# Optimization experiments

Measured on AMD Instinct MI355X. Metric: run time of the kernel, lower is better.

## Reference

```python
import jax, jax.numpy as jnp
import numpy as np

HEADS = 16
NUM_LANDMARKS = 64
PINV_ITERS = 6
D_MODEL = 1024


def _moore_penrose_pinv(x, num_iters):
    # Newton-Schulz iteration: V <- 0.25*V @ (13I - KV @ (15I - KV @ (7I - KV)))
    m = x.shape[-1]
    I = jnp.eye(m, dtype=x.dtype)
    V = x
    for _ in range(num_iters):
        KV = x @ V  # [..., m, m]
        V = 0.25 * V @ (13.0 * I - KV @ (15.0 * I - KV @ (7.0 * I - KV)))
    return V


def setup_inputs() -> dict:
    key = jax.random.key(0)
    k1, k2, k3 = jax.random.split(key, 3)
    b, n, d = 4, 4096, D_MODEL
    hidden_states = jax.random.normal(k1, (b, n, d), dtype=jnp.float32)
    Wqkv = jax.random.normal(k2, (d, 3 * d), dtype=jnp.float32) * 0.02
    bqkv = jnp.zeros((3 * d,), dtype=jnp.float32)
    Wout = jax.random.normal(k3, (d, d), dtype=jnp.float32) * 0.02
    bout = jnp.zeros((d,), dtype=jnp.float32)
    return {"hidden_states": hidden_states, "Wqkv": Wqkv, "bqkv": bqkv,
            "Wout": Wout, "bout": bout}


def reference(hidden_states, Wqkv, bqkv, Wout, bout):
    b, n, d = hidden_states.shape
    h, m = HEADS, NUM_LANDMARKS
    dh = d // h
    scale = 1.0 / np.sqrt(dh).astype(np.float32)
    # n is a multiple of m by construction, so the torch padding branch is a no-op.
    l = n // m  # tokens per landmark group

    qkv = hidden_states @ Wqkv + bqkv  # [b, n, 3d]
    q, k, v = jnp.split(qkv, 3, axis=-1)

    def to_heads(t):  # [b, n, d] -> [b, h, n, dh]
        return t.reshape(b, n, h, dh).transpose(0, 2, 1, 3)

    q, k, v = to_heads(q), to_heads(k), to_heads(v)
    q = q * scale

    # Landmarks: mean over contiguous groups of l tokens (sum / l in original).
    q_l = q.reshape(b, h, m, l, dh).mean(axis=3)  # [b, h, m, dh]
    k_l = k.reshape(b, h, m, l, dh).mean(axis=3)

    sim1 = jnp.einsum('bhid,bhjd->bhij', q, k_l)    # [b, h, n, m]
    sim2 = jnp.einsum('bhid,bhjd->bhij', q_l, k_l)  # [b, h, m, m]
    sim3 = jnp.einsum('bhid,bhjd->bhij', q_l, k)    # [b, h, m, n]

    attn1 = jax.nn.softmax(sim1, axis=-1)
    attn2 = jax.nn.softmax(sim2, axis=-1)
    attn3 = jax.nn.softmax(sim3, axis=-1)

    attn2_inv = _moore_penrose_pinv(attn2, PINV_ITERS)

    # out = attn1 @ attn2_inv @ (attn3 @ v), cheapest association
    out = attn1 @ (attn2_inv @ (attn3 @ v))  # [b, h, n, dh]
    out = out.transpose(0, 2, 1, 3).reshape(b, n, d)
    out = out @ Wout + bout
    return out
```

## Files before the change

kernel.cpp:

```cpp
#include <hip/hip_runtime.h>
#include <cstdint>

typedef unsigned short u16;
typedef __attribute__((ext_vector_type(8))) short s16x8;
typedef __attribute__((ext_vector_type(4))) float f32x4;

#define NTOK 4096
#define DH   64
#define DM   1024
#define NH   16

static __device__ __forceinline__ float b2f(u16 u){ return __uint_as_float(((unsigned)u)<<16); }
static __device__ __forceinline__ u16 f2b(float f){
  unsigned u = __float_as_uint(f);
  return (u16)((u + 0x7FFFu + ((u>>16)&1u)) >> 16);
}

static __device__ __forceinline__ void gload_lds16(const void* g, void* l) {
  __builtin_amdgcn_global_load_lds(
      (const __attribute__((address_space(1))) unsigned*)(uintptr_t)g,
      (__attribute__((address_space(3))) unsigned*)(uintptr_t)l, 16, 0, 0);
}

static __device__ __forceinline__ s16x8 ld8(const u16* p){ return *(const s16x8*)(const void*)p; }

__global__ __launch_bounds__(256) void k_cvt_xl(const float* __restrict__ hs, u16* __restrict__ Xb,
                                                float* __restrict__ Xl) {
  const int grp = blockIdx.x;
  const int d = blockIdx.y*256 + threadIdx.x;
  const float* p = hs + (long)grp*64*DM + d;
  u16* xo = Xb + (long)grp*64*DM + d;
  float s = 0.f;
  #pragma unroll 8
  for (int i = 0; i < 64; ++i) {
    const float v = p[(long)i*DM];
    s += v;
    xo[(long)i*DM] = f2b(v);
  }
  Xl[(long)grp*DM + d] = s * (1.0f/64.0f);
}

__global__ __launch_bounds__(256) void k_cvt_t(const float* __restrict__ in, u16* __restrict__ out, int R, int C) {
  __shared__ float tile[64][65];
  const int tc = blockIdx.x, tr = blockIdx.y;
  const int t = threadIdx.x, cx = t & 63, ry = t >> 6;
  #pragma unroll
  for (int p = 0; p < 16; ++p) {
    const int row = p*4 + ry;
    tile[row][cx] = in[(long)(tr*64 + row)*C + tc*64 + cx];
  }
  __syncthreads();
  #pragma unroll
  for (int p = 0; p < 16; ++p) {
    const int orow = p*4 + ry;
    out[(long)(tc*64 + orow)*R + tr*64 + cx] = f2b(tile[cx][orow]);
  }
}

__global__ __launch_bounds__(256) void k_lproj2(const float* __restrict__ Xl, const float* __restrict__ Wqkv,
                                                float* __restrict__ psum) {
  __shared__ __align__(16) float Xs[32][68];
  const int t = threadIdx.x;
  const int wcol = blockIdx.x*256 + t;
  const int r0 = blockIdx.y*32;
  const int kbase = blockIdx.z*128;
  float acc[32];
  #pragma unroll
  for (int r = 0; r < 32; ++r) acc[r] = 0.f;
  for (int k0 = kbase; k0 < kbase + 128; k0 += 64) {
    __syncthreads();
    for (int idx = t; idx < 2048; idx += 256)
      Xs[idx>>6][idx&63] = Xl[(long)(r0 + (idx>>6))*DM + k0 + (idx&63)];
    __syncthreads();
    for (int kk = 0; kk < 64; kk += 4) {
      f32x4 wv;
      #pragma unroll
      for (int j = 0; j < 4; ++j) wv[j] = Wqkv[(long)(k0+kk+j)*3072 + wcol];
      #pragma unroll
      for (int r = 0; r < 32; ++r) {
        const f32x4 xv = *(const f32x4*)&Xs[r][kk];
        acc[r] += xv[0]*wv[0] + xv[1]*wv[1] + xv[2]*wv[2] + xv[3]*wv[3];
      }
    }
  }
  float* po = psum + ((long)blockIdx.z*256 + r0)*2048 + wcol;
  #pragma unroll
  for (int r = 0; r < 32; ++r) po[(long)r*2048] = acc[r];
}

__global__ __launch_bounds__(256) void k_lreduce(const float* __restrict__ psum, const float* __restrict__ bqkv,
                                                 float* __restrict__ qlf, float* __restrict__ klf,
                                                 u16* __restrict__ qlb, u16* __restrict__ klb) {
  const long idx = (long)blockIdx.x*256 + threadIdx.x;
  const int row = (int)(idx >> 11), col = (int)(idx & 2047);
  float s = 0.f;
  #pragma unroll
  for (int z = 0; z < 8; ++z) s += psum[((long)z*256 + row)*2048 + col];
  const int isq = (col < 1024) ? 1 : 0;
  float val = s + bqkv[col];
  if (isq) val *= 0.125f;
  const int b = row >> 6, lm = row & 63;
  const int c2 = col & 1023, h = c2 >> 6, dh = c2 & 63;
  const long o = (((long)b*NH + h)*64 + lm)*64 + dh;
  if (isq) { qlf[o] = val; qlb[o] = f2b(val); }
  else     { klf[o] = val; klb[o] = f2b(val); }
}

template<int EPI>
__global__ __launch_bounds__(512, 2) void k_gemm256(
    const u16* __restrict__ A, const u16* __restrict__ Bt, const float* __restrict__ bias,
    int N, float* __restrict__ outF, u16* __restrict__ outQ, u16* __restrict__ outK, u16* __restrict__ outV)
{
  __shared__ __align__(16) u16 lds[4*16384];
  const int K = 1024;
  const int t = threadIdx.x;
  const int lane = t & 63;
  const int wid = t >> 6;
  const int c = lane & 15, g = lane >> 4;
  const int wm = wid >> 2, wn = wid & 3;
  const int fid = blockIdx.y*64 + blockIdx.x;
  const int nbx = ((fid & 7) << 3) | ((fid >> 3) & 7);
  const int nby = fid >> 6;
  const long arow0 = (long)nbx * 256;
  const long brow0 = (long)nby * 256;
  char* ldsb = (char*)lds;

  const int srow = t >> 2;
  const int schunk = (t & 3) ^ ((srow >> 1) & 3);
  const u16* gA0 = A  + (arow0 + srow)*K       + schunk*8;
  const u16* gA1 = A  + (arow0 + 128 + srow)*K + schunk*8;
  const u16* gB0 = Bt + (brow0 + srow)*K       + schunk*8;
  const u16* gB1 = Bt + (brow0 + 128 + srow)*K + schunk*8;
  const int dstoff = t*16;

#define STAGE_A(kt) { char* bse = ldsb + ((kt)&3)*32768; \
    gload_lds16(gA0 + (kt)*32, bse + dstoff); \
    gload_lds16(gA1 + (kt)*32, bse + 8192 + dstoff); }
#define STAGE_B(kt) { char* bse = ldsb + ((kt)&3)*32768 + 16384; \
    gload_lds16(gB0 + (kt)*32, bse + dstoff); \
    gload_lds16(gB1 + (kt)*32, bse + 8192 + dstoff); }

  const int gs = g ^ ((c >> 1) & 3);
  int aoff[2][4], boff[4];
  #pragma unroll
  for (int mi = 0; mi < 4; ++mi) {
    aoff[0][mi] = (0*128 + wm*64 + mi*16 + c)*64 + gs*16;
    aoff[1][mi] = (1*128 + wm*64 + mi*16 + c)*64 + gs*16;
    boff[mi]    = 16384 + (wn*64 + mi*16 + c)*64 + gs*16;
  }

  f32x4 acc0[4][4] = {};
  f32x4 acc1[4][4] = {};

  STAGE_A(0); STAGE_B(0); STAGE_A(1); STAGE_B(1); STAGE_A(2); STAGE_B(2);
  asm volatile("s_waitcnt vmcnt(8)" ::: "memory");
  __builtin_amdgcn_s_barrier();

  s16x8 af[4], bfr[4], af2[4];
  #pragma unroll
  for (int mi = 0; mi < 4; ++mi) af[mi]  = *(const s16x8*)(ldsb + aoff[0][mi]);
  #pragma unroll
  for (int ni = 0; ni < 4; ++ni) bfr[ni] = *(const s16x8*)(ldsb + boff[ni]);

  for (int kt = 0; kt < 32; ++kt) {
    char* buf  = ldsb + (kt&3)*32768;
    char* bufn = ldsb + ((kt+1)&3)*32768;
    if (kt + 3 < 32) { STAGE_A(kt+3) STAGE_B(kt+3) }
    asm volatile("s_waitcnt lgkmcnt(0)" ::: "memory");
    __builtin_amdgcn_sched_barrier(0);
    #pragma unroll
    for (int mi = 0; mi < 4; ++mi) af2[mi] = *(const s16x8*)(buf + aoff[1][mi]);
    __builtin_amdgcn_sched_barrier(0);
    __builtin_amdgcn_s_setprio(1);
    #pragma unroll
    for (int mi = 0; mi < 4; ++mi)
      #pragma unroll
      for (int ni = 0; ni < 4; ++ni)
        acc0[mi][ni] = __builtin_amdgcn_mfma_f32_16x16x32_bf16(af[mi], bfr[ni], acc0[mi][ni], 0, 0, 0);
    __builtin_amdgcn_s_setprio(0);
    asm volatile("s_waitcnt lgkmcnt(0)" ::: "memory");
    __builtin_amdgcn_sched_barrier(0);
    if (kt <= 28)      { asm volatile("s_waitcnt vmcnt(8)" ::: "memory"); }
    else if (kt == 29) { asm volatile("s_waitcnt vmcnt(4)" ::: "memory"); }
    else if (kt == 30) { asm volatile("s_waitcnt vmcnt(0)" ::: "memory"); }
    if (kt < 31) __builtin_amdgcn_s_barrier();
    s16x8 nf[4], nb[4];
    if (kt < 31) {
      #pragma unroll
      for (int mi = 0; mi < 4; ++mi) nf[mi] = *(const s16x8*)(bufn + aoff[0][mi]);
      #pragma unroll
      for (int ni = 0; ni < 4; ++ni) nb[ni] = *(const s16x8*)(bufn + boff[ni]);
    }
    __builtin_amdgcn_sched_barrier(0);
    __builtin_amdgcn_s_setprio(1);
    #pragma unroll
    for (int mi = 0; mi < 4; ++mi)
      #pragma unroll
      for (int ni = 0; ni < 4; ++ni)
        acc1[mi][ni] = __builtin_amdgcn_mfma_f32_16x16x32_bf16(af2[mi], bfr[ni], acc1[mi][ni], 0, 0, 0);
    __builtin_amdgcn_s_setprio(0);
    if (kt < 31) {
      #pragma unroll
      for (int mi = 0; mi < 4; ++mi) { af[mi] = nf[mi]; bfr[mi] = nb[mi]; }
    }
  }
#undef STAGE_A
#undef STAGE_B

  if (EPI == 0) {
    const int tensor = (int)(brow0 >> 10);
    u16* dst = (tensor == 0) ? outQ : (tensor == 1) ? outK : outV;
    const float mul = (tensor == 0) ? 0.125f : 1.0f;
    #pragma unroll
    for (int ph = 0; ph < 2; ++ph)
      #pragma unroll
      for (int mi = 0; mi < 4; ++mi) {
        const int rowb = ph*128 + wm*64 + mi*16 + g*4;
        #pragma unroll
        for (int ni = 0; ni < 4; ++ni) {
          const long gcol = brow0 + wn*64 + ni*16 + c;
          const int c2 = (int)(gcol & 1023);
          const int head = c2 >> 6, dh = c2 & 63;
          const float bv = bias[gcol];
          const f32x4 a = ph ? acc1[mi][ni] : acc0[mi][ni];
          #pragma unroll
          for (int r = 0; r < 4; ++r) {
            const long grow = arow0 + rowb + r;
            const int b = (int)(grow >> 12), tok = (int)(grow & 4095);
            dst[(((long)b*NH + head)*NTOK + tok)*DH + dh] = f2b((a[r] + bv)*mul);
          }
        }
      }
  } else {
    #pragma unroll
    for (int ph = 0; ph < 2; ++ph)
      #pragma unroll
      for (int mi = 0; mi < 4; ++mi) {
        const int rowb = ph*128 + wm*64 + mi*16 + g*4;
        #pragma unroll
        for (int ni = 0; ni < 4; ++ni) {
          const long gcol = brow0 + wn*64 + ni*16 + c;
          const float bv = bias[gcol];
          const f32x4 a = ph ? acc1[mi][ni] : acc0[mi][ni];
          #pragma unroll
          for (int r = 0; r < 4; ++r) {
            const long grow = arow0 + rowb + r;
            outF[grow*N + gcol] = a[r] + bv;
          }
        }
      }
  }
}

__global__ __launch_bounds__(256) void k_vtrans(const u16* __restrict__ v, u16* __restrict__ vt) {
  __shared__ u16 tile[64][65];
  const int bh = blockIdx.x >> 6, tt = blockIdx.x & 63;
  const int t = threadIdx.x, cx = t & 63, ry = t >> 6;
  const u16* vp = v + ((long)bh*NTOK + tt*64)*DH;
  #pragma unroll
  for (int p = 0; p < 16; ++p) { const int row = p*4 + ry; tile[row][cx] = vp[row*DH + cx]; }
  __syncthreads();
  u16* op = vt + (long)bh*DH*NTOK + tt*64;
  #pragma unroll
  for (int p = 0; p < 16; ++p) { const int orow = p*4 + ry; op[(long)orow*NTOK + cx] = tile[cx][orow]; }
}

#define PST 68
static __device__ __forceinline__ void mm_nn8(const float* A, const float* B, float* C, int t) {
  const int lane = t & 63, j0 = (t >> 6) << 3;
  float acc[8];
  #pragma unroll
  for (int j = 0; j < 8; ++j) acc[j] = 0.f;
  for (int k = 0; k < 64; k += 4) {
    const f32x4 a4 = *(const f32x4*)&A[lane*PST + k];
    #pragma unroll
    for (int dk = 0; dk < 4; ++dk) {
      const float a = a4[dk];
      const float* br = &B[(k + dk)*PST + j0];
      const f32x4 b0 = *(const f32x4*)(br);
      const f32x4 b1 = *(const f32x4*)(br + 4);
      #pragma unroll
      for (int qq = 0; qq < 4; ++qq) { acc[qq] += a*b0[qq]; acc[4+qq] += a*b1[qq]; }
    }
  }
  #pragma unroll
  for (int j = 0; j < 8; ++j) C[lane*PST + j0 + j] = acc[j];
}
static __device__ __forceinline__ void mm_nt8(const float* A, const float* B, float* C, int t) {
  const int lane = t & 63, j0 = (t >> 6) << 3;
  float acc[8];
  #pragma unroll
  for (int j = 0; j < 8; ++j) acc[j] = 0.f;
  for (int k = 0; k < 64; k += 4) {
    const f32x4 a4 = *(const f32x4*)&A[lane*PST + k];
    #pragma unroll
    for (int jj = 0; jj < 8; ++jj) {
      const f32x4 b4 = *(const f32x4*)&B[(j0 + jj)*PST + k];
      acc[jj] += a4[0]*b4[0] + a4[1]*b4[1] + a4[2]*b4[2] + a4[3]*b4[3];
    }
  }
  #pragma unroll
  for (int j = 0; j < 8; ++j) C[lane*PST + j0 + j] = acc[j];
}

__global__ __launch_bounds__(512) void k_pinv(const float* __restrict__ qlf, const float* __restrict__ klf,
                                              float* __restrict__ a2inv) {
  __shared__ __align__(16) float Xb[64*PST];
  __shared__ __align__(16) float Vb[64*PST];
  __shared__ __align__(16) float T1[64*PST];
  __shared__ __align__(16) float T2[64*PST];
  __shared__ __align__(16) float T3[64*PST];
  const int bh = blockIdx.x, t = threadIdx.x;
  const float* ql = qlf + (long)bh*4096;
  const float* kl = klf + (long)bh*4096;
  for (int i = t; i < 4096; i += 512) { T1[(i>>6)*PST + (i&63)] = ql[i]; T2[(i>>6)*PST + (i&63)] = kl[i]; }
  __syncthreads();
  mm_nt8(T1, T2, Xb, t);
  __syncthreads();
  if (t < 64) {
    float mx = -1e30f;
    for (int j = 0; j < 64; ++j) mx = fmaxf(mx, Xb[t*PST + j]);
    float s = 0.f;
    for (int j = 0; j < 64; ++j) { const float e = expf(Xb[t*PST + j] - mx); Xb[t*PST + j] = e; s += e; }
    const float inv = 1.0f/s;
    for (int j = 0; j < 64; ++j) Xb[t*PST + j] *= inv;
  }
  __syncthreads();
  for (int i = t; i < 4096; i += 512) { const int r = i>>6, cc = i&63; Vb[r*PST+cc] = Xb[r*PST+cc]; }
  __syncthreads();
  for (int it = 0; it < 6; ++it) {
    mm_nn8(Xb, Vb, T1, t);  __syncthreads();
    for (int i = t; i < 4096; i += 512) { const int r=i>>6, cc=i&63; T2[r*PST+cc] = (r==cc?7.0f:0.0f) - T1[r*PST+cc]; }
    __syncthreads();
    mm_nn8(T1, T2, T3, t);  __syncthreads();
    for (int i = t; i < 4096; i += 512) { const int r=i>>6, cc=i&63; T2[r*PST+cc] = (r==cc?15.0f:0.0f) - T3[r*PST+cc]; }
    __syncthreads();
    mm_nn8(T1, T2, T3, t);  __syncthreads();
    for (int i = t; i < 4096; i += 512) { const int r=i>>6, cc=i&63; T2[r*PST+cc] = (r==cc?13.0f:0.0f) - T3[r*PST+cc]; }
    __syncthreads();
    mm_nn8(Vb, T2, T3, t);  __syncthreads();
    for (int i = t; i < 4096; i += 512) { const int r=i>>6, cc=i&63; Vb[r*PST+cc] = 0.25f*T3[r*PST+cc]; }
    __syncthreads();
  }
  for (int i = t; i < 4096; i += 512) a2inv[(long)bh*4096 + i] = Vb[(i>>6)*PST + (i&63)];
}

__global__ __launch_bounds__(256) void k_attn3v_p(const u16* __restrict__ qlb, const u16* __restrict__ kk,
                                                  const u16* __restrict__ vt,
                                                  float* __restrict__ zp, float* __restrict__ sp) {
  __shared__ __align__(16) float Zl[4][64][64];
  __shared__ float Sl[4][64];
  __shared__ __align__(16) u16 Pl[4][64][40];
  const int bh = blockIdx.x >> 2, qt = blockIdx.x & 3;
  const int t = threadIdx.x, w = t >> 6, lane = t & 63;
  const int c = lane & 15, g = lane >> 4;

  s16x8 aq[4][2];
  const u16* qlp = qlb + (long)bh*4096;
  #pragma unroll
  for (int mi = 0; mi < 4; ++mi)
    #pragma unroll
    for (int ks = 0; ks < 2; ++ks)
      aq[mi][ks] = ld8(qlp + (mi*16 + c)*64 + ks*32 + g*8);

  f32x4 zacc[4][4] = {};
  float sl[4][4] = {};
  const u16* kp = kk + (long)bh*NTOK*DH;
  const u16* vp = vt + (long)bh*DH*NTOK;
  char* pbase = (char*)&Pl[w][0][0];
  const int tok00 = qt*1024 + w*256;

  for (int it = 0; it < 8; ++it) {
    const int t0 = tok00 + it*32;
    f32x4 sacc[4][2] = {};
    s16x8 kb[2][2];
    #pragma unroll
    for (int cg = 0; cg < 2; ++cg)
      #pragma unroll
      for (int ks = 0; ks < 2; ++ks)
        kb[cg][ks] = ld8(kp + (long)(t0 + cg*16 + c)*64 + ks*32 + g*8);
    #pragma unroll
    for (int cg = 0; cg < 2; ++cg)
      #pragma unroll
      for (int ks = 0; ks < 2; ++ks)
        #pragma unroll
        for (int mi = 0; mi < 4; ++mi)
          sacc[mi][cg] = __builtin_amdgcn_mfma_f32_16x16x32_bf16(aq[mi][ks], kb[cg][ks], sacc[mi][cg], 0, 0, 0);
    #pragma unroll
    for (int mi = 0; mi < 4; ++mi)
      #pragma unroll
      for (int r = 0; r < 4; ++r) {
        const int row = mi*16 + g*4 + r;
        const float p0 = __expf(sacc[mi][0][r]);
        const float p1 = __expf(sacc[mi][1][r]);
        sl[mi][r] += p0 + p1;
        char* base = pbase + row*80;
        *(u16*)(base + c*2)      = f2b(p0);
        *(u16*)(base + 32 + c*2) = f2b(p1);
      }
    s16x8 pa[4];
    #pragma unroll
    for (int mi = 0; mi < 4; ++mi) pa[mi] = *(const s16x8*)(pbase + (mi*16 + c)*80 + g*16);
    #pragma unroll
    for (int ni = 0; ni < 4; ++ni) {
      const s16x8 vb = ld8(vp + (long)(ni*16 + c)*NTOK + t0 + g*8);
      #pragma unroll
      for (int mi = 0; mi < 4; ++mi)
        zacc[mi][ni] = __builtin_amdgcn_mfma_f32_16x16x32_bf16(pa[mi], vb, zacc[mi][ni], 0, 0, 0);
    }
  }
  #pragma unroll
  for (int mi = 0; mi < 4; ++mi)
    #pragma unroll
    for (int r = 0; r < 4; ++r) {
      float s = sl[mi][r];
      s += __shfl_xor(s, 1); s += __shfl_xor(s, 2); s += __shfl_xor(s, 4); s += __shfl_xor(s, 8);
      sl[mi][r] = s;
    }
  #pragma unroll
  for (int mi = 0; mi < 4; ++mi)
    #pragma unroll
    for (int ni = 0; ni < 4; ++ni)
      #pragma unroll
      for (int r = 0; r < 4; ++r)
        Zl[w][mi*16 + g*4 + r][ni*16 + c] = zacc[mi][ni][r];
  if (c == 0)
    #pragma unroll
    for (int mi = 0; mi < 4; ++mi)
      #pragma unroll
      for (int r = 0; r < 4; ++r)
        Sl[w][mi*16 + g*4 + r] = sl[mi][r];
  __syncthreads();
  float* zpp = zp + (long)blockIdx.x*4096;
  for (int i = t; i < 4096; i += 256) {
    const int row = i >> 6, dh = i & 63;
    zpp[i] = Zl[0][row][dh] + Zl[1][row][dh] + Zl[2][row][dh] + Zl[3][row][dh];
  }
  if (t < 64) sp[(long)blockIdx.x*64 + t] = Sl[0][t] + Sl[1][t] + Sl[2][t] + Sl[3][t];
}

__global__ __launch_bounds__(512) void k_w2(const float* __restrict__ a2inv,
                                            const float* __restrict__ zp, const float* __restrict__ sp,
                                            u16* __restrict__ w2t) {
  __shared__ __align__(16) float Ai[64*PST];
  __shared__ __align__(16) float Zi[64*PST];
  __shared__ __align__(16) float Ci[64*PST];
  __shared__ float Ss[64];
  const int bh = blockIdx.x, t = threadIdx.x;
  if (t < 64) {
    float ss = 0.f;
    #pragma unroll
    for (int qt = 0; qt < 4; ++qt) ss += sp[(long)(bh*4 + qt)*64 + t];
    Ss[t] = 1.0f / ss;
  }
  for (int i = t; i < 4096; i += 512)
    Ai[(i>>6)*PST + (i&63)] = a2inv[(long)bh*4096 + i];
  __syncthreads();
  for (int i = t; i < 4096; i += 512) {
    float zs = 0.f;
    #pragma unroll
    for (int qt = 0; qt < 4; ++qt) zs += zp[((long)(bh*4 + qt))*4096 + i];
    Zi[(i>>6)*PST + (i&63)] = zs * Ss[i>>6];
  }
  __syncthreads();
  mm_nn8(Ai, Zi, Ci, t);
  __syncthreads();
  for (int i = t; i < 4096; i += 512) { const int r = i>>6, cc = i&63; w2t[(long)bh*4096 + cc*64 + r] = f2b(Ci[r*PST + cc]); }
}

#define P1ST 144
__global__ __launch_bounds__(256) void k_attn1(const u16* __restrict__ q, const u16* __restrict__ klb,
                                               const u16* __restrict__ w2t, u16* __restrict__ ao) {
  __shared__ __align__(16) u16 Pl[4][64][72];
  const int bx = blockIdx.x, bh = bx >> 4, tt = bx & 15;
  const int b = bh >> 4, h = bh & 15;
  const int t = threadIdx.x, w = t >> 6, lane = t & 63;
  const int c = lane & 15, g = lane >> 4;
  const int tok0 = tt*256 + w*64;
  const u16* qp  = q + ((long)bh*NTOK + tok0)*DH;
  const u16* klp = klb + (long)bh*4096;
  const u16* wp  = w2t + (long)bh*4096;
  char* pbase = (char*)&Pl[w][0][0];

  s16x8 aq[4][2], kb[4][2], wb[4][2];
  #pragma unroll
  for (int i = 0; i < 4; ++i)
    #pragma unroll
    for (int ks = 0; ks < 2; ++ks) {
      aq[i][ks] = ld8(qp + (long)(i*16 + c)*DH + ks*32 + g*8);
      kb[i][ks] = ld8(klp + (i*16 + c)*64 + ks*32 + g*8);
      wb[i][ks] = ld8(wp  + (i*16 + c)*64 + ks*32 + g*8);
    }
  f32x4 sacc[4][4] = {};
  #pragma unroll
  for (int ks = 0; ks < 2; ++ks)
    #pragma unroll
    for (int mi = 0; mi < 4; ++mi)
      #pragma unroll
      for (int ni = 0; ni < 4; ++ni)
        sacc[mi][ni] = __builtin_amdgcn_mfma_f32_16x16x32_bf16(aq[mi][ks], kb[ni][ks], sacc[mi][ni], 0, 0, 0);

  float rs[4][4];
  #pragma unroll
  for (int mi = 0; mi < 4; ++mi)
    #pragma unroll
    for (int r = 0; r < 4; ++r) {
      const int row = mi*16 + g*4 + r;
      char* base = pbase + row*P1ST;
      float ssum = 0.f;
      #pragma unroll
      for (int ni = 0; ni < 4; ++ni) {
        const float p = __expf(sacc[mi][ni][r]);
        ssum += p;
        *(u16*)(base + (ni*16 + c)*2) = f2b(p);
      }
      ssum += __shfl_xor(ssum, 1); ssum += __shfl_xor(ssum, 2);
      ssum += __shfl_xor(ssum, 4); ssum += __shfl_xor(ssum, 8);
      rs[mi][r] = ssum;
    }
  __builtin_amdgcn_s_barrier();
  s16x8 pa[4][2];
  #pragma unroll
  for (int mi = 0; mi < 4; ++mi)
    #pragma unroll
    for (int ks = 0; ks < 2; ++ks)
      pa[mi][ks] = *(const s16x8*)(pbase + (mi*16 + c)*P1ST + ks*64 + g*16);
  f32x4 oacc[4][4] = {};
  #pragma unroll
  for (int ks = 0; ks < 2; ++ks)
    #pragma unroll
    for (int mi = 0; mi < 4; ++mi)
      #pragma unroll
      for (int ni = 0; ni < 4; ++ni)
        oacc[mi][ni] = __builtin_amdgcn_mfma_f32_16x16x32_bf16(pa[mi][ks], wb[ni][ks], oacc[mi][ni], 0, 0, 0);

  u16* op = ao + (long)b*NTOK*DM + (long)h*64;
  #pragma unroll
  for (int mi = 0; mi < 4; ++mi)
    #pragma unroll
    for (int r = 0; r < 4; ++r) {
      const int tok = tok0 + mi*16 + g*4 + r;
      const float inv = 1.0f / rs[mi][r];
      #pragma unroll
      for (int ni = 0; ni < 4; ++ni)
        op[(long)tok*DM + ni*16 + c] = f2b(oacc[mi][ni][r] * inv);
    }
}

extern "C" void kernel_launch(void* const* d_in, const int* in_sizes, int n_in,
                              void* d_out, int out_size, void* d_ws, size_t ws_size,
                              hipStream_t stream) {
  const float* hs   = (const float*)d_in[0];
  const float* Wqkv = (const float*)d_in[1];
  const float* bqkv = (const float*)d_in[2];
  const float* Wout = (const float*)d_in[3];
  const float* bout = (const float*)d_in[4];
  float* out = (float*)d_out;
  char* w = (char*)d_ws;

  u16*  Xb    = (u16*)(w);
  float* zp   = (float*)(w);
  float* sp   = (float*)(w + 4194304L);
  u16*  WqkvT = (u16*)(w + 33554432L);
  u16*  WoutT = (u16*)(w + 39845888L);
  u16*  q     = (u16*)(w + 41943040L);
  float* psum = (float*)(w + 41943040L);
  u16*  k     = (u16*)(w + 75497472L);
  u16*  v     = (u16*)(w + 109051904L);
  u16*  vt    = (u16*)(w + 142606336L);
  float* Xl   = (float*)(w + 142606336L);
  float* qlf  = (float*)(w + 176160768L);
  float* klf  = (float*)(w + 177209344L);
  u16*  qlb   = (u16*)(w + 178257920L);
  u16*  klb   = (u16*)(w + 178782208L);
  float* a2i  = (float*)(w + 179306496L);
  u16*  w2t   = (u16*)(w + 181403648L);
  u16*  ao    = (u16*)(w + 181927936L);

  k_cvt_xl<<<dim3(256,4), 256, 0, stream>>>(hs, Xb, Xl);
  k_cvt_t<<<dim3(48,16), 256, 0, stream>>>(Wqkv, WqkvT, 1024, 3072);
  k_cvt_t<<<dim3(16,16), 256, 0, stream>>>(Wout, WoutT, 1024, 1024);
  k_lproj2<<<dim3(8,8,8), 256, 0, stream>>>(Xl, Wqkv, psum);
  k_lreduce<<<2048, 256, 0, stream>>>(psum, bqkv, qlf, klf, qlb, klb);
  k_gemm256<0><<<dim3(64,12), 512, 0, stream>>>(Xb, WqkvT, bqkv, 3072, nullptr, q, k, v);
  k_vtrans<<<4096, 256, 0, stream>>>(v, vt);
  k_pinv<<<64, 512, 0, stream>>>(qlf, klf, a2i);
  k_attn3v_p<<<256, 256, 0, stream>>>(qlb, k, vt, zp, sp);
  k_w2<<<64, 512, 0, stream>>>(a2i, zp, sp, w2t);
  k_attn1<<<1024, 256, 0, stream>>>(q, klb, w2t, ao);
  k_gemm256<1><<<dim3(64,4), 512, 0, stream>>>(ao, WoutT, bout, 1024, out, nullptr, nullptr, nullptr);
}
```

Measured before the change: 367.6 us.

## Fuse preprocessing kernels, write V transposed from GEMM, co-schedule pinv with attn3

Merges the hidden-state conversion and both weight transposes into one launch. The QKV GEMM epilogue now writes V already transposed through LDS, which removes the separate transpose kernel and one round trip of V through memory. The pinv blocks and a finer-split attn3·V pass (8 token chunks per head) now share one launch, so the serial pinv work overlaps with the attention reduction. k_w2 is widened to 1024 threads to match. This adds LDS pressure and branch divergence between block roles, and the pinv blocks still set the critical path.

```diff
diff --git a/kernel.cpp b/kernel.cpp
--- a/kernel.cpp
+++ b/kernel.cpp
@@ -24,26 +24,31 @@
 
 static __device__ __forceinline__ s16x8 ld8(const u16* p){ return *(const s16x8*)(const void*)p; }
 
-__global__ __launch_bounds__(256) void k_cvt_xl(const float* __restrict__ hs, u16* __restrict__ Xb,
-                                                float* __restrict__ Xl) {
-  const int grp = blockIdx.x;
-  const int d = blockIdx.y*256 + threadIdx.x;
-  const float* p = hs + (long)grp*64*DM + d;
-  u16* xo = Xb + (long)grp*64*DM + d;
-  float s = 0.f;
-  #pragma unroll 8
-  for (int i = 0; i < 64; ++i) {
-    const float v = p[(long)i*DM];
-    s += v;
-    xo[(long)i*DM] = f2b(v);
-  }
-  Xl[(long)grp*DM + d] = s * (1.0f/64.0f);
-}
-
-__global__ __launch_bounds__(256) void k_cvt_t(const float* __restrict__ in, u16* __restrict__ out, int R, int C) {
+__global__ __launch_bounds__(256) void k_pre(const float* __restrict__ hs, u16* __restrict__ Xb,
+                                             float* __restrict__ Xl,
+                                             const float* __restrict__ Wqkv, u16* __restrict__ WqkvT,
+                                             const float* __restrict__ Wout, u16* __restrict__ WoutT) {
   __shared__ float tile[64][65];
-  const int tc = blockIdx.x, tr = blockIdx.y;
-  const int t = threadIdx.x, cx = t & 63, ry = t >> 6;
+  const int bid = blockIdx.x, t = threadIdx.x;
+  if (bid < 1024) {
+    const int grp = bid >> 2;
+    const int d = (bid & 3)*256 + t;
+    const float* p = hs + (long)grp*64*DM + d;
+    u16* xo = Xb + (long)grp*64*DM + d;
+    float s = 0.f;
+    #pragma unroll 8
+    for (int i = 0; i < 64; ++i) {
+      const float v = p[(long)i*DM];
+      s += v;
+      xo[(long)i*DM] = f2b(v);
+    }
+    Xl[(long)grp*DM + d] = s * (1.0f/64.0f);
+    return;
+  }
+  const float* in; u16* out; int R, C, tc, tr;
+  if (bid < 1792) { const int x = bid - 1024; in = Wqkv; out = WqkvT; R = 1024; C = 3072; tc = x % 48; tr = x / 48; }
+  else            { const int x = bid - 1792; in = Wout; out = WoutT; R = 1024; C = 1024; tc = x & 15;  tr = x >> 4; }
+  const int cx = t & 63, ry = t >> 6;
   #pragma unroll
   for (int p = 0; p < 16; ++p) {
     const int row = p*4 + ry;
@@ -209,28 +214,62 @@
 
   if (EPI == 0) {
     const int tensor = (int)(brow0 >> 10);
-    u16* dst = (tensor == 0) ? outQ : (tensor == 1) ? outK : outV;
-    const float mul = (tensor == 0) ? 0.125f : 1.0f;
-    #pragma unroll
-    for (int ph = 0; ph < 2; ++ph)
-      #pragma unroll
-      for (int mi = 0; mi < 4; ++mi) {
-        const int rowb = ph*128 + wm*64 + mi*16 + g*4;
-        #pragma unroll
-        for (int ni = 0; ni < 4; ++ni) {
-          const long gcol = brow0 + wn*64 + ni*16 + c;
-          const int c2 = (int)(gcol & 1023);
-          const int head = c2 >> 6, dh = c2 & 63;
-          const float bv = bias[gcol];
-          const f32x4 a = ph ? acc1[mi][ni] : acc0[mi][ni];
+    if (tensor == 2) {
+      __syncthreads();
+      u16* wlds = lds + wid*4224;
+      const int hbase = (int)((brow0 + wn*64) & 1023);
+      const int head = hbase >> 6;
+      #pragma unroll
+      for (int ph = 0; ph < 2; ++ph) {
+        const long grow0 = arow0 + ph*128 + wm*64;
+        const int b = (int)(grow0 >> 12), tok0r = (int)(grow0 & 4095);
+        #pragma unroll
+        for (int mi = 0; mi < 4; ++mi)
           #pragma unroll
-          for (int r = 0; r < 4; ++r) {
-            const long grow = arow0 + rowb + r;
-            const int b = (int)(grow >> 12), tok = (int)(grow & 4095);
-            dst[(((long)b*NH + head)*NTOK + tok)*DH + dh] = f2b((a[r] + bv)*mul);
+          for (int ni = 0; ni < 4; ++ni) {
+            const float bv = bias[brow0 + wn*64 + ni*16 + c];
+            const f32x4 a = ph ? acc1[mi][ni] : acc0[mi][ni];
+            #pragma unroll
+            for (int r = 0; r < 4; ++r)
+              wlds[(mi*16 + g*4 + r)*66 + ni*16 + c] = f2b(a[r] + bv);
+          }
+        asm volatile("s_waitcnt lgkmcnt(0)" ::: "memory");
+        u16* vbase = outV + (((long)b*NH + head)*DH)*NTOK + tok0r;
+        #pragma unroll
+        for (int j = 0; j < 8; ++j) {
+          const int d = j*8 + (lane >> 3);
+          const int tk = (lane & 7)*8;
+          s16x8 vv;
+          #pragma unroll
+          for (int s2 = 0; s2 < 8; ++s2) vv[s2] = (short)wlds[(tk + s2)*66 + d];
+          *(s16x8*)(vbase + (long)d*NTOK + tk) = vv;
+        }
+        asm volatile("s_waitcnt lgkmcnt(0)" ::: "memory");
+      }
+    } else {
+      u16* dst = (tensor == 0) ? outQ : outK;
+      const float mul = (tensor == 0) ? 0.125f : 1.0f;
+      #pragma unroll
+      for (int ph = 0; ph < 2; ++ph)
+        #pragma unroll
+        for (int mi = 0; mi < 4; ++mi) {
+          const int rowb = ph*128 + wm*64 + mi*16 + g*4;
+          #pragma unroll
+          for (int ni = 0; ni < 4; ++ni) {
+            const long gcol = brow0 + wn*64 + ni*16 + c;
+            const int c2 = (int)(gcol & 1023);
+            const int head = c2 >> 6, dh = c2 & 63;
+            const float bv = bias[gcol];
+            const f32x4 a = ph ? acc1[mi][ni] : acc0[mi][ni];
+            #pragma unroll
+            for (int r = 0; r < 4; ++r) {
+              const long grow = arow0 + rowb + r;
+              const int b = (int)(grow >> 12), tok = (int)(grow & 4095);
+              dst[(((long)b*NH + head)*NTOK + tok)*DH + dh] = f2b((a[r] + bv)*mul);
+            }
           }
         }
-      }
+    }
   } else {
     #pragma unroll
     for (int ph = 0; ph < 2; ++ph)
@@ -252,19 +291,6 @@
   }
 }
 
-__global__ __launch_bounds__(256) void k_vtrans(const u16* __restrict__ v, u16* __restrict__ vt) {
-  __shared__ u16 tile[64][65];
-  const int bh = blockIdx.x >> 6, tt = blockIdx.x & 63;
-  const int t = threadIdx.x, cx = t & 63, ry = t >> 6;
-  const u16* vp = v + ((long)bh*NTOK + tt*64)*DH;
-  #pragma unroll
-  for (int p = 0; p < 16; ++p) { const int row = p*4 + ry; tile[row][cx] = vp[row*DH + cx]; }
-  __syncthreads();
-  u16* op = vt + (long)bh*DH*NTOK + tt*64;
-  #pragma unroll
-  for (int p = 0; p < 16; ++p) { const int orow = p*4 + ry; op[(long)orow*NTOK + cx] = tile[cx][orow]; }
-}
-
 #define PST 68
 static __device__ __forceinline__ void mm_nn8(const float* A, const float* B, float* C, int t) {
   const int lane = t & 63, j0 = (t >> 6) << 3;
@@ -302,146 +328,164 @@
   #pragma unroll
   for (int j = 0; j < 8; ++j) C[lane*PST + j0 + j] = acc[j];
 }
-
-__global__ __launch_bounds__(512) void k_pinv(const float* __restrict__ qlf, const float* __restrict__ klf,
-                                              float* __restrict__ a2inv) {
-  __shared__ __align__(16) float Xb[64*PST];
-  __shared__ __align__(16) float Vb[64*PST];
-  __shared__ __align__(16) float T1[64*PST];
-  __shared__ __align__(16) float T2[64*PST];
-  __shared__ __align__(16) float T3[64*PST];
-  const int bh = blockIdx.x, t = threadIdx.x;
-  const float* ql = qlf + (long)bh*4096;
-  const float* kl = klf + (long)bh*4096;
-  for (int i = t; i < 4096; i += 512) { T1[(i>>6)*PST + (i&63)] = ql[i]; T2[(i>>6)*PST + (i&63)] = kl[i]; }
+static __device__ __forceinline__ void mm_nn4(const float* A, const float* B, float* C, int t) {
+  const int lane = t & 63, j0 = (t >> 6) << 2;
+  float acc[4] = {0.f, 0.f, 0.f, 0.f};
+  for (int k = 0; k < 64; k += 4) {
+    const f32x4 a4 = *(const f32x4*)&A[lane*PST + k];
+    #pragma unroll
+    for (int dk = 0; dk < 4; ++dk) {
+      const f32x4 b0 = *(const f32x4*)&B[(k + dk)*PST + j0];
+      #pragma unroll
+      for (int q = 0; q < 4; ++q) acc[q] += a4[dk]*b0[q];
+    }
+  }
+  #pragma unroll
+  for (int j = 0; j < 4; ++j) C[lane*PST + j0 + j] = acc[j];
+}
+
+__global__ __launch_bounds__(512) void k_pa(const float* __restrict__ qlf, const float* __restrict__ klf,
+                                            float* __restrict__ a2inv,
+                                            const u16* __restrict__ qlb, const u16* __restrict__ kk,
+                                            const u16* __restrict__ vt,
+                                            float* __restrict__ zp, float* __restrict__ sp) {
+  __shared__ __align__(16) char smem[87040];
+  const int t = threadIdx.x;
+  if (blockIdx.x < 64) {
+    float* Xb = (float*)smem;
+    float* Vb = Xb + 64*PST;
+    float* T1 = Vb + 64*PST;
+    float* T2 = T1 + 64*PST;
+    float* T3 = T2 + 64*PST;
+    const int bh = blockIdx.x;
+    const float* ql = qlf + (long)bh*4096;
+    const float* kl = klf + (long)bh*4096;
+    for (int i = t; i < 4096; i += 512) { T1[(i>>6)*PST + (i&63)] = ql[i]; T2[(i>>6)*PST + (i&63)] = kl[i]; }
+    __syncthreads();
+    mm_nt8(T1, T2, Xb, t);
+    __syncthreads();
+    if (t < 64) {
+      float mx = -1e30f;
+      for (int j = 0; j < 64; ++j) mx = fmaxf(mx, Xb[t*PST + j]);
+      float s = 0.f;
+      for (int j = 0; j < 64; ++j) { const float e = expf(Xb[t*PST + j] - mx); Xb[t*PST + j] = e; s += e; }
+      const float inv = 1.0f/s;
+      for (int j = 0; j < 64; ++j) Xb[t*PST + j] *= inv;
+    }
+    __syncthreads();
+    for (int i = t; i < 4096; i += 512) { const int r = i>>6, cc = i&63; Vb[r*PST+cc] = Xb[r*PST+cc]; }
+    __syncthreads();
+    for (int it = 0; it < 6; ++it) {
+      mm_nn8(Xb, Vb, T1, t);  __syncthreads();
+      for (int i = t; i < 4096; i += 512) { const int r=i>>6, cc=i&63; T2[r*PST+cc] = (r==cc?7.0f:0.0f) - T1[r*PST+cc]; }
+      __syncthreads();
+      mm_nn8(T1, T2, T3, t);  __syncthreads();
+      for (int i = t; i < 4096; i += 512) { const int r=i>>6, cc=i&63; T2[r*PST+cc] = (r==cc?15.0f:0.0f) - T3[r*PST+cc]; }
+      __syncthreads();
+      mm_nn8(T1, T2, T3, t);  __syncthreads();
+      for (int i = t; i < 4096; i += 512) { const int r=i>>6, cc=i&63; T2[r*PST+cc] = (r==cc?13.0f:0.0f) - T3[r*PST+cc]; }
+      __syncthreads();
+      mm_nn8(Vb, T2, T3, t);  __syncthreads();
+      for (int i = t; i < 4096; i += 512) { const int r=i>>6, cc=i&63; Vb[r*PST+cc] = 0.25f*T3[r*PST+cc]; }
+      __syncthreads();
+    }
+    for (int i = t; i < 4096; i += 512) a2inv[(long)bh*4096 + i] = Vb[(i>>6)*PST + (i&63)];
+    return;
+  }
+  float* Zlp = (float*)smem;
+  float* Slp = (float*)(smem + 65536);
+  char*  Plb = smem + 66560;
+  const int abid = blockIdx.x - 64;
+  const int bh = abid >> 3, qt = abid & 7;
+  if (t < 256) {
+    const int w = t >> 6, lane = t & 63;
+    const int c = lane & 15, g = lane >> 4;
+    s16x8 aq[4][2];
+    const u16* qlp = qlb + (long)bh*4096;
+    #pragma unroll
+    for (int mi = 0; mi < 4; ++mi)
+      #pragma unroll
+      for (int ks = 0; ks < 2; ++ks)
+        aq[mi][ks] = ld8(qlp + (mi*16 + c)*64 + ks*32 + g*8);
+
+    f32x4 zacc[4][4] = {};
+    float sl[4][4] = {};
+    const u16* kp = kk + (long)bh*NTOK*DH;
+    const u16* vp = vt + (long)bh*DH*NTOK;
+    char* pbase = Plb + w*5120;
+    const int tok00 = qt*512 + w*128;
+
+    for (int it = 0; it < 4; ++it) {
+      const int t0 = tok00 + it*32;
+      f32x4 sacc[4][2] = {};
+      s16x8 kb[2][2];
+      #pragma unroll
+      for (int cg = 0; cg < 2; ++cg)
+        #pragma unroll
+        for (int ks = 0; ks < 2; ++ks)
+          kb[cg][ks] = ld8(kp + (long)(t0 + cg*16 + c)*64 + ks*32 + g*8);
+      #pragma unroll
+      for (int cg = 0; cg < 2; ++cg)
+        #pragma unroll
+        for (int ks = 0; ks < 2; ++ks)
+          #pragma unroll
+          for (int mi = 0; mi < 4; ++mi)
+            sacc[mi][cg] = __builtin_amdgcn_mfma_f32_16x16x32_bf16(aq[mi][ks], kb[cg][ks], sacc[mi][cg], 0, 0, 0);
+      #pragma unroll
+      for (int mi = 0; mi < 4; ++mi)
+        #pragma unroll
+        for (int r = 0; r < 4; ++r) {
+          const int row = mi*16 + g*4 + r;
+          const float p0 = __expf(sacc[mi][0][r]);
+          const float p1 = __expf(sacc[mi][1][r]);
+          sl[mi][r] += p0 + p1;
+          char* base = pbase + row*80;
+          *(u16*)(base + c*2)      = f2b(p0);
+          *(u16*)(base + 32 + c*2) = f2b(p1);
+        }
+      s16x8 pa[4];
+      #pragma unroll
+      for (int mi = 0; mi < 4; ++mi) pa[mi] = *(const s16x8*)(pbase + (mi*16 + c)*80 + g*16);
+      #pragma unroll
+      for (int ni = 0; ni < 4; ++ni) {
+        const s16x8 vb = ld8(vp + (long)(ni*16 + c)*NTOK + t0 + g*8);
+        #pragma unroll
+        for (int mi = 0; mi < 4; ++mi)
+          zacc[mi][ni] = __builtin_amdgcn_mfma_f32_16x16x32_bf16(pa[mi], vb, zacc[mi][ni], 0, 0, 0);
+      }
+    }
+    #pragma unroll
+    for (int mi = 0; mi < 4; ++mi)
+      #pragma unroll
+      for (int r = 0; r < 4; ++r) {
+        float s = sl[mi][r];
+        s += __shfl_xor(s, 1); s += __shfl_xor(s, 2); s += __shfl_xor(s, 4); s += __shfl_xor(s, 8);
+        sl[mi][r] = s;
+      }
+    #pragma unroll
+    for (int mi = 0; mi < 4; ++mi)
+      #pragma unroll
+      for (int ni = 0; ni < 4; ++ni)
+        #pragma unroll
+        for (int r = 0; r < 4; ++r)
+          Zlp[w*4096 + (mi*16 + g*4 + r)*64 + ni*16 + c] = zacc[mi][ni][r];
+    if (c == 0)
+      #pragma unroll
+      for (int mi = 0; mi < 4; ++mi)
+        #pragma unroll
+        for (int r = 0; r < 4; ++r)
+          Slp[w*64 + mi*16 + g*4 + r] = sl[mi][r];
+  }
   __syncthreads();
-  mm_nt8(T1, T2, Xb, t);
-  __syncthreads();
-  if (t < 64) {
-    float mx = -1e30f;
-    for (int j = 0; j < 64; ++j) mx = fmaxf(mx, Xb[t*PST + j]);
-    float s = 0.f;
-    for (int j = 0; j < 64; ++j) { const float e = expf(Xb[t*PST + j] - mx); Xb[t*PST + j] = e; s += e; }
-    const float inv = 1.0f/s;
-    for (int j = 0; j < 64; ++j) Xb[t*PST + j] *= inv;
-  }
-  __syncthreads();
-  for (int i = t; i < 4096; i += 512) { const int r = i>>6, cc = i&63; Vb[r*PST+cc] = Xb[r*PST+cc]; }
-  __syncthreads();
-  for (int it = 0; it < 6; ++it) {
-    mm_nn8(Xb, Vb, T1, t);  __syncthreads();
-    for (int i = t; i < 4096; i += 512) { const int r=i>>6, cc=i&63; T2[r*PST+cc] = (r==cc?7.0f:0.0f) - T1[r*PST+cc]; }
-    __syncthreads();
-    mm_nn8(T1, T2, T3, t);  __syncthreads();
-    for (int i = t; i < 4096; i += 512) { const int r=i>>6, cc=i&63; T2[r*PST+cc] = (r==cc?15.0f:0.0f) - T3[r*PST+cc]; }
-    __syncthreads();
-    mm_nn8(T1, T2, T3, t);  __syncthreads();
-    for (int i = t; i < 4096; i += 512) { const int r=i>>6, cc=i&63; T2[r*PST+cc] = (r==cc?13.0f:0.0f) - T3[r*PST+cc]; }
-    __syncthreads();
-    mm_nn8(Vb, T2, T3, t);  __syncthreads();
-    for (int i = t; i < 4096; i += 512) { const int r=i>>6, cc=i&63; Vb[r*PST+cc] = 0.25f*T3[r*PST+cc]; }
-    __syncthreads();
-  }
-  for (int i = t; i < 4096; i += 512) a2inv[(long)bh*4096 + i] = Vb[(i>>6)*PST + (i&63)];
-}
-
-__global__ __launch_bounds__(256) void k_attn3v_p(const u16* __restrict__ qlb, const u16* __restrict__ kk,
-                                                  const u16* __restrict__ vt,
-                                                  float* __restrict__ zp, float* __restrict__ sp) {
-  __shared__ __align__(16) float Zl[4][64][64];
-  __shared__ float Sl[4][64];
-  __shared__ __align__(16) u16 Pl[4][64][40];
-  const int bh = blockIdx.x >> 2, qt = blockIdx.x & 3;
-  const int t = threadIdx.x, w = t >> 6, lane = t & 63;
-  const int c = lane & 15, g = lane >> 4;
-
-  s16x8 aq[4][2];
-  const u16* qlp = qlb + (long)bh*4096;
-  #pragma unroll
-  for (int mi = 0; mi < 4; ++mi)
-    #pragma unroll
-    for (int ks = 0; ks < 2; ++ks)
-      aq[mi][ks] = ld8(qlp + (mi*16 + c)*64 + ks*32 + g*8);
-
-  f32x4 zacc[4][4] = {};
-  float sl[4][4] = {};
-  const u16* kp = kk + (long)bh*NTOK*DH;
-  const u16* vp = vt + (long)bh*DH*NTOK;
-  char* pbase = (char*)&Pl[w][0][0];
-  const int tok00 = qt*1024 + w*256;
-
-  for (int it = 0; it < 8; ++it) {
-    const int t0 = tok00 + it*32;
-    f32x4 sacc[4][2] = {};
-    s16x8 kb[2][2];
-    #pragma unroll
-    for (int cg = 0; cg < 2; ++cg)
-      #pragma unroll
-      for (int ks = 0; ks < 2; ++ks)
-        kb[cg][ks] = ld8(kp + (long)(t0 + cg*16 + c)*64 + ks*32 + g*8);
-    #pragma unroll
-    for (int cg = 0; cg < 2; ++cg)
-      #pragma unroll
-      for (int ks = 0; ks < 2; ++ks)
-        #pragma unroll
-        for (int mi = 0; mi < 4; ++mi)
-          sacc[mi][cg] = __builtin_amdgcn_mfma_f32_16x16x32_bf16(aq[mi][ks], kb[cg][ks], sacc[mi][cg], 0, 0, 0);
-    #pragma unroll
-    for (int mi = 0; mi < 4; ++mi)
-      #pragma unroll
-      for (int r = 0; r < 4; ++r) {
-        const int row = mi*16 + g*4 + r;
-        const float p0 = __expf(sacc[mi][0][r]);
-        const float p1 = __expf(sacc[mi][1][r]);
-        sl[mi][r] += p0 + p1;
-        char* base = pbase + row*80;
-        *(u16*)(base + c*2)      = f2b(p0);
-        *(u16*)(base + 32 + c*2) = f2b(p1);
-      }
-    s16x8 pa[4];
-    #pragma unroll
-    for (int mi = 0; mi < 4; ++mi) pa[mi] = *(const s16x8*)(pbase + (mi*16 + c)*80 + g*16);
-    #pragma unroll
-    for (int ni = 0; ni < 4; ++ni) {
-      const s16x8 vb = ld8(vp + (long)(ni*16 + c)*NTOK + t0 + g*8);
-      #pragma unroll
-      for (int mi = 0; mi < 4; ++mi)
-        zacc[mi][ni] = __builtin_amdgcn_mfma_f32_16x16x32_bf16(pa[mi], vb, zacc[mi][ni], 0, 0, 0);
-    }
-  }
-  #pragma unroll
-  for (int mi = 0; mi < 4; ++mi)
-    #pragma unroll
-    for (int r = 0; r < 4; ++r) {
-      float s = sl[mi][r];
-      s += __shfl_xor(s, 1); s += __shfl_xor(s, 2); s += __shfl_xor(s, 4); s += __shfl_xor(s, 8);
-      sl[mi][r] = s;
-    }
-  #pragma unroll
-  for (int mi = 0; mi < 4; ++mi)
-    #pragma unroll
-    for (int ni = 0; ni < 4; ++ni)
-      #pragma unroll
-      for (int r = 0; r < 4; ++r)
-        Zl[w][mi*16 + g*4 + r][ni*16 + c] = zacc[mi][ni][r];
-  if (c == 0)
-    #pragma unroll
-    for (int mi = 0; mi < 4; ++mi)
-      #pragma unroll
-      for (int r = 0; r < 4; ++r)
-        Sl[w][mi*16 + g*4 + r] = sl[mi][r];
-  __syncthreads();
-  float* zpp = zp + (long)blockIdx.x*4096;
-  for (int i = t; i < 4096; i += 256) {
-    const int row = i >> 6, dh = i & 63;
-    zpp[i] = Zl[0][row][dh] + Zl[1][row][dh] + Zl[2][row][dh] + Zl[3][row][dh];
-  }
-  if (t < 64) sp[(long)blockIdx.x*64 + t] = Sl[0][t] + Sl[1][t] + Sl[2][t] + Sl[3][t];
-}
-
-__global__ __launch_bounds__(512) void k_w2(const float* __restrict__ a2inv,
-                                            const float* __restrict__ zp, const float* __restrict__ sp,
-                                            u16* __restrict__ w2t) {
+  float* zpp = zp + (long)abid*4096;
+  for (int i = t; i < 4096; i += 512)
+    zpp[i] = Zlp[i] + Zlp[4096 + i] + Zlp[8192 + i] + Zlp[12288 + i];
+  if (t < 64) sp[(long)abid*64 + t] = Slp[t] + Slp[64 + t] + Slp[128 + t] + Slp[192 + t];
+}
+
+__global__ __launch_bounds__(1024) void k_w2(const float* __restrict__ a2inv,
+                                             const float* __restrict__ zp, const float* __restrict__ sp,
+                                             u16* __restrict__ w2t) {
   __shared__ __align__(16) float Ai[64*PST];
   __shared__ __align__(16) float Zi[64*PST];
   __shared__ __align__(16) float Ci[64*PST];
@@ -450,22 +494,22 @@
   if (t < 64) {
     float ss = 0.f;
     #pragma unroll
-    for (int qt = 0; qt < 4; ++qt) ss += sp[(long)(bh*4 + qt)*64 + t];
+    for (int qt = 0; qt < 8; ++qt) ss += sp[(long)(bh*8 + qt)*64 + t];
     Ss[t] = 1.0f / ss;
   }
-  for (int i = t; i < 4096; i += 512)
+  for (int i = t; i < 4096; i += 1024)
     Ai[(i>>6)*PST + (i&63)] = a2inv[(long)bh*4096 + i];
   __syncthreads();
-  for (int i = t; i < 4096; i += 512) {
+  for (int i = t; i < 4096; i += 1024) {
     float zs = 0.f;
     #pragma unroll
-    for (int qt = 0; qt < 4; ++qt) zs += zp[((long)(bh*4 + qt))*4096 + i];
+    for (int qt = 0; qt < 8; ++qt) zs += zp[((long)(bh*8 + qt))*4096 + i];
     Zi[(i>>6)*PST + (i&63)] = zs * Ss[i>>6];
   }
   __syncthreads();
-  mm_nn8(Ai, Zi, Ci, t);
+  mm_nn4(Ai, Zi, Ci, t);
   __syncthreads();
-  for (int i = t; i < 4096; i += 512) { const int r = i>>6, cc = i&63; w2t[(long)bh*4096 + cc*64 + r] = f2b(Ci[r*PST + cc]); }
+  for (int i = t; i < 4096; i += 1024) { const int r = i>>6, cc = i&63; w2t[(long)bh*4096 + cc*64 + r] = f2b(Ci[r*PST + cc]); }
 }
 
 #define P1ST 144
@@ -560,15 +604,14 @@
 
   u16*  Xb    = (u16*)(w);
   float* zp   = (float*)(w);
-  float* sp   = (float*)(w + 4194304L);
+  float* sp   = (float*)(w + 8388608L);
   u16*  WqkvT = (u16*)(w + 33554432L);
   u16*  WoutT = (u16*)(w + 39845888L);
   u16*  q     = (u16*)(w + 41943040L);
   float* psum = (float*)(w + 41943040L);
   u16*  k     = (u16*)(w + 75497472L);
-  u16*  v     = (u16*)(w + 109051904L);
+  float* Xl   = (float*)(w + 109051904L);
   u16*  vt    = (u16*)(w + 142606336L);
-  float* Xl   = (float*)(w + 142606336L);
   float* qlf  = (float*)(w + 176160768L);
   float* klf  = (float*)(w + 177209344L);
   u16*  qlb   = (u16*)(w + 178257920L);
@@ -577,16 +620,12 @@
   u16*  w2t   = (u16*)(w + 181403648L);
   u16*  ao    = (u16*)(w + 181927936L);
 
-  k_cvt_xl<<<dim3(256,4), 256, 0, stream>>>(hs, Xb, Xl);
-  k_cvt_t<<<dim3(48,16), 256, 0, stream>>>(Wqkv, WqkvT, 1024, 3072);
-  k_cvt_t<<<dim3(16,16), 256, 0, stream>>>(Wout, WoutT, 1024, 1024);
+  k_pre<<<2048, 256, 0, stream>>>(hs, Xb, Xl, Wqkv, WqkvT, Wout, WoutT);
   k_lproj2<<<dim3(8,8,8), 256, 0, stream>>>(Xl, Wqkv, psum);
   k_lreduce<<<2048, 256, 0, stream>>>(psum, bqkv, qlf, klf, qlb, klb);
-  k_gemm256<0><<<dim3(64,12), 512, 0, stream>>>(Xb, WqkvT, bqkv, 3072, nullptr, q, k, v);
-  k_vtrans<<<4096, 256, 0, stream>>>(v, vt);
-  k_pinv<<<64, 512, 0, stream>>>(qlf, klf, a2i);
-  k_attn3v_p<<<256, 256, 0, stream>>>(qlb, k, vt, zp, sp);
-  k_w2<<<64, 512, 0, stream>>>(a2i, zp, sp, w2t);
+  k_gemm256<0><<<dim3(64,12), 512, 0, stream>>>(Xb, WqkvT, bqkv, 3072, nullptr, q, k, vt);
+  k_pa<<<576, 512, 0, stream>>>(qlf, klf, a2i, qlb, k, vt, zp, sp);
+  k_w2<<<64, 1024, 0, stream>>>(a2i, zp, sp, w2t);
   k_attn1<<<1024, 256, 0, stream>>>(q, klb, w2t, ao);
   k_gemm256<1><<<dim3(64,4), 512, 0, stream>>>(ao, WoutT, bout, 1024, out, nullptr, nullptr, nullptr);
 }
```

Measured after the change: 334.6 us. -9.0%, faster.
